# Kernel tuning notes

Hardware: AMD Instinct MI355X
Metric: run time of the kernel (lower is better)

Reference implementation:

```python
import jax, jax.numpy as jnp
import numpy as np

N_NODES = 100000
N_EDGES = 1600000
IN_FEATURES = 256
OUT_FEATURES = 64


def setup_inputs() -> dict:
    key = jax.random.key(0)
    k_x, k_r, k_c, k_v, k_w = jax.random.split(key, 5)
    x = jax.random.normal(k_x, (N_NODES, IN_FEATURES), dtype=jnp.float32)
    adj_rows = jax.random.randint(k_r, (N_EDGES,), 0, N_NODES, dtype=jnp.int64)
    adj_cols = jax.random.randint(k_c, (N_EDGES,), 0, N_NODES, dtype=jnp.int64)
    adj_vals = jax.random.uniform(k_v, (N_EDGES,), dtype=jnp.float32)
    # Glorot-uniform init as in reset_parameters()
    init_range = np.sqrt(6.0 / (IN_FEATURES + OUT_FEATURES)).astype(np.float32)
    W = jax.random.uniform(k_w, (IN_FEATURES, OUT_FEATURES), dtype=jnp.float32,
                           minval=-init_range, maxval=init_range)
    return {"x": x, "adj_rows": adj_rows, "adj_cols": adj_cols,
            "adj_vals": adj_vals, "W": W}


def reference(x, adj_rows, adj_cols, adj_vals, W):
    # support = x @ W  : dense [N, in] x [in, out]
    support = x @ W  # [N, out]
    # output = adj @ support : COO SpMM via gather + segment-sum
    # msgs[e] = adj_vals[e] * support[col[e]]
    msgs = adj_vals[:, None] * support[adj_cols]  # [E, out]
    output = jax.ops.segment_sum(msgs, adj_rows, num_segments=N_NODES)  # [N, out]
    return output
```

## Files before the change

kernel.cpp:

```cpp
#include <hip/hip_runtime.h>


#define KDIM 256
#define MDIM 64
#define BSHIFT 7
#define BMAX 1024
#define FCAP 6500

__device__ __forceinline__ void gld_lds16(const float* g, float* l) {
    __builtin_amdgcn_global_load_lds(
        (const __attribute__((address_space(1))) unsigned int*)g,
        (__attribute__((address_space(3))) unsigned int*)l, 16, 0, 0);
}

__global__ __launch_bounds__(256, 3) void gemm_xw(
    const float* __restrict__ x, const float* __restrict__ W,
    float* __restrict__ support, int nrows)
{
    __shared__ float lds[2][5120];
    const int tid  = threadIdx.x;
    const int lane = tid & 63;
    const int wid  = tid >> 6;
    const int rg   = tid >> 3;
    const int fg   = tid & 7;
    const int r0   = rg * 8;
    const int f0   = fg * 8;
    const int sk   = rg & 3;
    const int row0 = blockIdx.x * 256;

    float acc[8][8];
    #pragma unroll
    for (int i = 0; i < 8; ++i)
        #pragma unroll
        for (int j = 0; j < 8; ++j) acc[i][j] = 0.f;

    auto stage = [&](int bf, int kt) {
        #pragma unroll
        for (int j = 0; j < 4; ++j) {
            const int ig  = wid * 4 + j;
            const int row = ig * 16 + (lane >> 2);
            const int kq  = (lane & 3) ^ ((row >> 3) & 3);
            const int gr  = min(row0 + row, nrows - 1);
            gld_lds16(x + (size_t)gr * KDIM + kt + kq * 4,
                      &lds[bf][ig * 256]);
        }
        {
            const int kk = wid * 4 + (lane >> 4);
            const int fq = lane & 15;
            gld_lds16(W + (size_t)(kt + kk) * MDIM + fq * 4,
                      &lds[bf][4096 + wid * 256]);
        }
    };

    auto compute = [&](int bf) {
        const float* xs = &lds[bf][0];
        const float* ws = &lds[bf][4096];
        #pragma unroll
        for (int q = 0; q < 4; ++q) {
            float4 xv[8];
            const int slot = q ^ sk;
            #pragma unroll
            for (int i = 0; i < 8; ++i)
                xv[i] = *reinterpret_cast<const float4*>(
                            &xs[(r0 + i) * 16 + slot * 4]);
            #pragma unroll
            for (int k2 = 0; k2 < 4; ++k2) {
                const int kk = q * 4 + k2;
                const float4 wa = *reinterpret_cast<const float4*>(
                                      &ws[kk * 64 + f0]);
                const float4 wb = *reinterpret_cast<const float4*>(
                                      &ws[kk * 64 + f0 + 4]);
                #pragma unroll
                for (int i = 0; i < 8; ++i) {
                    const float xk = (k2 == 0) ? xv[i].x :
                                     (k2 == 1) ? xv[i].y :
                                     (k2 == 2) ? xv[i].z : xv[i].w;
                    acc[i][0] = fmaf(xk, wa.x, acc[i][0]);
                    acc[i][1] = fmaf(xk, wa.y, acc[i][1]);
                    acc[i][2] = fmaf(xk, wa.z, acc[i][2]);
                    acc[i][3] = fmaf(xk, wa.w, acc[i][3]);
                    acc[i][4] = fmaf(xk, wb.x, acc[i][4]);
                    acc[i][5] = fmaf(xk, wb.y, acc[i][5]);
                    acc[i][6] = fmaf(xk, wb.z, acc[i][6]);
                    acc[i][7] = fmaf(xk, wb.w, acc[i][7]);
                }
            }
        }
    };

    stage(0, 0);
    __syncthreads();
    int bf = 0;
    #pragma unroll 1
    for (int t = 0; t < KDIM / 16; ++t) {
        if (t < KDIM / 16 - 1) stage(bf ^ 1, (t + 1) * 16);
        compute(bf);
        __syncthreads();
        bf ^= 1;
    }

    #pragma unroll
    for (int i = 0; i < 8; ++i) {
        const int grow = row0 + r0 + i;
        if (grow < nrows) {
            *reinterpret_cast<float4*>(&support[(size_t)grow * MDIM + f0]) =
                make_float4(acc[i][0], acc[i][1], acc[i][2], acc[i][3]);
            *reinterpret_cast<float4*>(&support[(size_t)grow * MDIM + f0 + 4]) =
                make_float4(acc[i][4], acc[i][5], acc[i][6], acc[i][7]);
        }
    }
}

__global__ __launch_bounds__(256) void coarse_hist(
    const int* __restrict__ rows, int* __restrict__ counts,
    int nedges, int nbuckets)
{
    __shared__ int lb[BMAX];
    const int t = threadIdx.x;
    for (int i = t; i < nbuckets; i += 256) lb[i] = 0;
    __syncthreads();
    int e = blockIdx.x * 256 + t;
    const int stride = gridDim.x * 256;
    for (; e < nedges; e += stride)
        atomicAdd(&lb[rows[e] >> BSHIFT], 1);
    __syncthreads();
    for (int i = t; i < nbuckets; i += 256) {
        int c = lb[i];
        if (c) atomicAdd(&counts[i], c);
    }
}

__global__ __launch_bounds__(256) void coarse_scan(
    const int* __restrict__ counts, int* __restrict__ offsets,
    int* __restrict__ cursor, int n)
{
    __shared__ int sh[256];
    const int t = threadIdx.x;
    const int base = t * 4;
    int v0 = 0, v1 = 0, v2 = 0, v3 = 0;
    if (base + 0 < n) v0 = counts[base + 0];
    if (base + 1 < n) v1 = counts[base + 1];
    if (base + 2 < n) v2 = counts[base + 2];
    if (base + 3 < n) v3 = counts[base + 3];
    const int tsum = v0 + v1 + v2 + v3;
    sh[t] = tsum;
    __syncthreads();
    for (int off = 1; off < 256; off <<= 1) {
        int xv = (t >= off) ? sh[t - off] : 0;
        __syncthreads();
        sh[t] += xv;
        __syncthreads();
    }
    int excl = sh[t] - tsum;
    if (base + 0 < n) { offsets[base + 0] = excl; cursor[base + 0] = excl; } excl += v0;
    if (base + 1 < n) { offsets[base + 1] = excl; cursor[base + 1] = excl; } excl += v1;
    if (base + 2 < n) { offsets[base + 2] = excl; cursor[base + 2] = excl; } excl += v2;
    if (base + 3 < n) { offsets[base + 3] = excl; cursor[base + 3] = excl; }
}

__global__ __launch_bounds__(256) void bin_edges(
    const int* __restrict__ rows, const int* __restrict__ cols,
    const float* __restrict__ vals, int* __restrict__ cursor,
    int2* __restrict__ edata, int nedges, int nbuckets)
{
    __shared__ int lb[BMAX];
    const int t = threadIdx.x;
    const int per = (nedges + gridDim.x - 1) / gridDim.x;
    const int e0 = blockIdx.x * per;
    const int e1 = min(e0 + per, nedges);

    for (int i = t; i < nbuckets; i += 256) lb[i] = 0;
    __syncthreads();
    for (int e = e0 + t; e < e1; e += 256)
        atomicAdd(&lb[rows[e] >> BSHIFT], 1);
    __syncthreads();
    for (int i = t; i < nbuckets; i += 256) {
        int c = lb[i];
        lb[i] = c ? atomicAdd(&cursor[i], c) : 0;
    }
    __syncthreads();
    for (int e = e0 + t; e < e1; e += 256) {
        const int r = rows[e];
        const int pos = atomicAdd(&lb[r >> BSHIFT], 1);
        int2 pk;
        pk.x = (cols[e] & 0x1FFFF) | ((r & 127) << 17);
        pk.y = __float_as_int(vals[e]);
        edata[pos] = pk;
    }
}

__global__ __launch_bounds__(256) void fine_scatter(
    const int* __restrict__ offsets, const int* __restrict__ counts,
    int2* __restrict__ edata, int* __restrict__ foff, int* __restrict__ fcnt,
    int* __restrict__ bflag, int nrows)
{
    __shared__ int2 lrec[FCAP];
    __shared__ int cnt[128];
    __shared__ int cur[128];
    __shared__ int sh[128];
    const int t = threadIdx.x;
    const int b = blockIdx.x;
    const int beg = offsets[b];
    const int cntE = counts[b];
    const int row0 = b << BSHIFT;

    if (t < 128) cnt[t] = 0;
    __syncthreads();

    if (cntE > FCAP) {
        if (t == 0) bflag[b] = 1;
        if (t < 128) {
            const int grow = row0 + t;
            if (grow < nrows) { foff[grow] = beg; fcnt[grow] = 0; }
        }
        return;
    }

    for (int k = t; k < cntE; k += 256) {
        int2 p = edata[beg + k];
        lrec[k] = p;
        atomicAdd(&cnt[(p.x >> 17) & 127], 1);
    }
    __syncthreads();

    if (t < 128) sh[t] = cnt[t];
    __syncthreads();
    for (int off = 1; off < 128; off <<= 1) {
        int xv = 0;
        if (t < 128 && t >= off) xv = sh[t - off];
        __syncthreads();
        if (t < 128) sh[t] += xv;
        __syncthreads();
    }
    if (t < 128) {
        const int excl = sh[t] - cnt[t];
        cur[t] = excl;
        const int grow = row0 + t;
        if (grow < nrows) { foff[grow] = beg + excl; fcnt[grow] = cnt[t]; }
    }
    __syncthreads();

    for (int k = t; k < cntE; k += 256) {
        const int2 p = lrec[k];
        const int rl = (p.x >> 17) & 127;
        const int pos = beg + atomicAdd(&cur[rl], 1);
        edata[pos] = make_int2(p.x & 0x1FFFF, p.y);
    }
}

__global__ __launch_bounds__(256) void spmm_reduce(
    const int* __restrict__ foff, const int* __restrict__ fcnt,
    const int2* __restrict__ edata, const float* __restrict__ support,
    float* __restrict__ out, int nrows)
{
    const int g = blockIdx.x * 16 + (threadIdx.x >> 4);
    const int f0 = (threadIdx.x & 15) * 4;
    if (g >= nrows) return;
    int e = foff[g];
    const int end = e + fcnt[g];
    float ax = 0.f, ay = 0.f, az = 0.f, aw = 0.f;

    for (; e + 8 <= end; e += 8) {
        int2 p[8];
        #pragma unroll
        for (int u = 0; u < 8; ++u) p[u] = edata[e + u];
        float4 s[8];
        #pragma unroll
        for (int u = 0; u < 8; ++u)
            s[u] = *reinterpret_cast<const float4*>(
                       &support[(size_t)p[u].x * MDIM + f0]);
        #pragma unroll
        for (int u = 0; u < 8; ++u) {
            const float v = __int_as_float(p[u].y);
            ax = fmaf(v, s[u].x, ax); ay = fmaf(v, s[u].y, ay);
            az = fmaf(v, s[u].z, az); aw = fmaf(v, s[u].w, aw);
        }
    }
    for (; e < end; ++e) {
        const int2 p = edata[e];
        const float v = __int_as_float(p.y);
        float4 s = *reinterpret_cast<const float4*>(
                       &support[(size_t)p.x * MDIM + f0]);
        ax = fmaf(v, s.x, ax); ay = fmaf(v, s.y, ay);
        az = fmaf(v, s.z, az); aw = fmaf(v, s.w, aw);
    }
    *reinterpret_cast<float4*>(&out[(size_t)g * MDIM + f0]) =
        make_float4(ax, ay, az, aw);
}

__global__ __launch_bounds__(256) void scatter_tail(
    const int* __restrict__ offsets, const int* __restrict__ counts,
    const int* __restrict__ bflag, const int2* __restrict__ edata,
    const float* __restrict__ support, float* __restrict__ out)
{
    const int b = blockIdx.x;
    if (!bflag[b]) return;
    const int beg = offsets[b];
    const int end = beg + counts[b];
    const int row0 = b << BSHIFT;
    const int g  = threadIdx.x >> 4;
    const int f0 = (threadIdx.x & 15) * 4;
    for (int e = beg + g; e < end; e += 16) {
        const int2 p = edata[e];
        const int c = p.x & 0x1FFFF;
        const int r = row0 + ((p.x >> 17) & 127);
        const float v = __int_as_float(p.y);
        float4 s = *reinterpret_cast<const float4*>(
                       &support[(size_t)c * MDIM + f0]);
        float* op = &out[(size_t)r * MDIM + f0];
        atomicAdd(op + 0, v * s.x);
        atomicAdd(op + 1, v * s.y);
        atomicAdd(op + 2, v * s.z);
        atomicAdd(op + 3, v * s.w);
    }
}

__global__ __launch_bounds__(256) void scatter_edges(
    const int* __restrict__ rows, const int* __restrict__ cols,
    const float* __restrict__ vals, const float* __restrict__ support,
    float* __restrict__ out, int nedges)
{
    const int t = blockIdx.x * blockDim.x + threadIdx.x;
    const int fq = (t & 15) * 4;
    int e = t >> 4;
    const int estride = (gridDim.x * blockDim.x) >> 4;
    for (; e < nedges; e += estride) {
        const int r = rows[e];
        const int c = cols[e];
        const float v = vals[e];
        float4 s = *reinterpret_cast<const float4*>(
                       &support[(size_t)c * MDIM + fq]);
        float* op = &out[(size_t)r * MDIM + fq];
        atomicAdd(op + 0, v * s.x);
        atomicAdd(op + 1, v * s.y);
        atomicAdd(op + 2, v * s.z);
        atomicAdd(op + 3, v * s.w);
    }
}

extern "C" void kernel_launch(void* const* d_in, const int* in_sizes, int n_in,
                              void* d_out, int out_size, void* d_ws, size_t ws_size,
                              hipStream_t stream) {
    const float* x    = (const float*)d_in[0];
    const int*   rows = (const int*)d_in[1];
    const int*   cols = (const int*)d_in[2];
    const float* vals = (const float*)d_in[3];
    const float* W    = (const float*)d_in[4];
    float* out = (float*)d_out;

    const int nnodes = in_sizes[0] / KDIM;
    const int nedges = in_sizes[1];
    const int nbuckets = (nnodes + 127) >> BSHIFT;

    auto align256 = [](size_t v) { return (v + 255) & ~(size_t)255; };
    const size_t sz_support = align256((size_t)nnodes * MDIM * 4);
    const size_t sz_bkt     = align256((size_t)BMAX * 4);
    const size_t sz_nodes   = align256((size_t)nnodes * 4);
    const size_t sz_edata   = align256((size_t)nedges * 8);
    const size_t need = sz_support + 4 * sz_bkt + 2 * sz_nodes + sz_edata;

    char* w = (char*)d_ws;
    float* support = (float*)w;  w += sz_support;

    gemm_xw<<<dim3((nnodes + 255) / 256), dim3(256), 0, stream>>>(
        x, W, support, nnodes);

    if (ws_size >= need && nbuckets <= BMAX && nnodes <= (1 << 17)) {
        int* counts  = (int*)w;  w += sz_bkt;
        int* offsets = (int*)w;  w += sz_bkt;
        int* cursor  = (int*)w;  w += sz_bkt;
        int* bflag   = (int*)w;  w += sz_bkt;
        int* foff    = (int*)w;  w += sz_nodes;
        int* fcnt    = (int*)w;  w += sz_nodes;
        int2* edata  = (int2*)w;

        hipMemsetAsync(counts, 0, (size_t)nbuckets * 4, stream);
        hipMemsetAsync(bflag, 0, (size_t)nbuckets * 4, stream);

        coarse_hist<<<dim3(256), dim3(256), 0, stream>>>(
            rows, counts, nedges, nbuckets);
        coarse_scan<<<dim3(1), dim3(256), 0, stream>>>(
            counts, offsets, cursor, nbuckets);
        bin_edges<<<dim3(256), dim3(256), 0, stream>>>(
            rows, cols, vals, cursor, edata, nedges, nbuckets);
        fine_scatter<<<dim3(nbuckets), dim3(256), 0, stream>>>(
            offsets, counts, edata, foff, fcnt, bflag, nnodes);
        spmm_reduce<<<dim3((nnodes + 15) / 16), dim3(256), 0, stream>>>(
            foff, fcnt, edata, support, out, nnodes);
        scatter_tail<<<dim3(nbuckets), dim3(256), 0, stream>>>(
            offsets, counts, bflag, edata, support, out);
    } else {
        hipMemsetAsync(d_out, 0, (size_t)out_size * sizeof(float), stream);
        scatter_edges<<<dim3(4096), dim3(256), 0, stream>>>(
            rows, cols, vals, support, out, nedges);
    }
}
```

Before: 391.5 us.

## Replace LDS-tiled GEMM with one-row-per-thread kernel reading W uniformly

The x@W kernel changes from a 256-thread, LDS double-buffered 8x8 register-tiled design to a 64-thread kernel where each thread computes one full output row of 64 values. Each thread loads its own x row directly with float4 loads and reads W through uniform addresses, which the compiler can turn into scalar loads. This removes the LDS staging and barriers, but each thread's x reads are strided by a full row, so loads across a wavefront are uncoalesced. It also needs 64 accumulators plus prefetch registers per thread, and W rows are re-read by every wave.

```diff
diff --git a/kernel.cpp b/kernel.cpp
--- a/kernel.cpp
+++ b/kernel.cpp
@@ -7,107 +7,51 @@
 #define BMAX 1024
 #define FCAP 6500
 
-__device__ __forceinline__ void gld_lds16(const float* g, float* l) {
-    __builtin_amdgcn_global_load_lds(
-        (const __attribute__((address_space(1))) unsigned int*)g,
-        (__attribute__((address_space(3))) unsigned int*)l, 16, 0, 0);
-}
-
-__global__ __launch_bounds__(256, 3) void gemm_xw(
+__global__ __launch_bounds__(64) void gemm_xw(
     const float* __restrict__ x, const float* __restrict__ W,
     float* __restrict__ support, int nrows)
 {
-    __shared__ float lds[2][5120];
-    const int tid  = threadIdx.x;
-    const int lane = tid & 63;
-    const int wid  = tid >> 6;
-    const int rg   = tid >> 3;
-    const int fg   = tid & 7;
-    const int r0   = rg * 8;
-    const int f0   = fg * 8;
-    const int sk   = rg & 3;
-    const int row0 = blockIdx.x * 256;
-
-    float acc[8][8];
+    const int row_raw = blockIdx.x * 64 + threadIdx.x;
+    const int row = min(row_raw, nrows - 1);
+    const float4* xr = reinterpret_cast<const float4*>(x + (size_t)row * KDIM);
+
+    float acc[MDIM];
     #pragma unroll
-    for (int i = 0; i < 8; ++i)
-        #pragma unroll
-        for (int j = 0; j < 8; ++j) acc[i][j] = 0.f;
-
-    auto stage = [&](int bf, int kt) {
-        #pragma unroll
-        for (int j = 0; j < 4; ++j) {
-            const int ig  = wid * 4 + j;
-            const int row = ig * 16 + (lane >> 2);
-            const int kq  = (lane & 3) ^ ((row >> 3) & 3);
-            const int gr  = min(row0 + row, nrows - 1);
-            gld_lds16(x + (size_t)gr * KDIM + kt + kq * 4,
-                      &lds[bf][ig * 256]);
+    for (int f = 0; f < MDIM; ++f) acc[f] = 0.f;
+
+    float4 xa0 = xr[0], xa1 = xr[1], xa2 = xr[2], xa3 = xr[3];
+
+    #pragma unroll 1
+    for (int kt = 0; kt < KDIM; kt += 16) {
+        float4 xb0, xb1, xb2, xb3;
+        if (kt + 16 < KDIM) {
+            const int nq = (kt >> 2) + 4;
+            xb0 = xr[nq + 0]; xb1 = xr[nq + 1];
+            xb2 = xr[nq + 2]; xb3 = xr[nq + 3];
         }
-        {
-            const int kk = wid * 4 + (lane >> 4);
-            const int fq = lane & 15;
-            gld_lds16(W + (size_t)(kt + kk) * MDIM + fq * 4,
-                      &lds[bf][4096 + wid * 256]);
-        }
-    };
-
-    auto compute = [&](int bf) {
-        const float* xs = &lds[bf][0];
-        const float* ws = &lds[bf][4096];
         #pragma unroll
         for (int q = 0; q < 4; ++q) {
-            float4 xv[8];
-            const int slot = q ^ sk;
+            const float4 xv = (q == 0) ? xa0 : (q == 1) ? xa1 :
+                              (q == 2) ? xa2 : xa3;
             #pragma unroll
-            for (int i = 0; i < 8; ++i)
-                xv[i] = *reinterpret_cast<const float4*>(
-                            &xs[(r0 + i) * 16 + slot * 4]);
-            #pragma unroll
-            for (int k2 = 0; k2 < 4; ++k2) {
-                const int kk = q * 4 + k2;
-                const float4 wa = *reinterpret_cast<const float4*>(
-                                      &ws[kk * 64 + f0]);
-                const float4 wb = *reinterpret_cast<const float4*>(
-                                      &ws[kk * 64 + f0 + 4]);
+            for (int j = 0; j < 4; ++j) {
+                const float xk = (j == 0) ? xv.x : (j == 1) ? xv.y :
+                                 (j == 2) ? xv.z : xv.w;
+                const float* wrow = &W[(size_t)(kt + q * 4 + j) * MDIM];
                 #pragma unroll
-                for (int i = 0; i < 8; ++i) {
-                    const float xk = (k2 == 0) ? xv[i].x :
-                                     (k2 == 1) ? xv[i].y :
-                                     (k2 == 2) ? xv[i].z : xv[i].w;
-                    acc[i][0] = fmaf(xk, wa.x, acc[i][0]);
-                    acc[i][1] = fmaf(xk, wa.y, acc[i][1]);
-                    acc[i][2] = fmaf(xk, wa.z, acc[i][2]);
-                    acc[i][3] = fmaf(xk, wa.w, acc[i][3]);
-                    acc[i][4] = fmaf(xk, wb.x, acc[i][4]);
-                    acc[i][5] = fmaf(xk, wb.y, acc[i][5]);
-                    acc[i][6] = fmaf(xk, wb.z, acc[i][6]);
-                    acc[i][7] = fmaf(xk, wb.w, acc[i][7]);
-                }
+                for (int f = 0; f < MDIM; ++f)
+                    acc[f] = fmaf(xk, wrow[f], acc[f]);
             }
         }
-    };
-
-    stage(0, 0);
-    __syncthreads();
-    int bf = 0;
-    #pragma unroll 1
-    for (int t = 0; t < KDIM / 16; ++t) {
-        if (t < KDIM / 16 - 1) stage(bf ^ 1, (t + 1) * 16);
-        compute(bf);
-        __syncthreads();
-        bf ^= 1;
-    }
-
-    #pragma unroll
-    for (int i = 0; i < 8; ++i) {
-        const int grow = row0 + r0 + i;
-        if (grow < nrows) {
-            *reinterpret_cast<float4*>(&support[(size_t)grow * MDIM + f0]) =
-                make_float4(acc[i][0], acc[i][1], acc[i][2], acc[i][3]);
-            *reinterpret_cast<float4*>(&support[(size_t)grow * MDIM + f0 + 4]) =
-                make_float4(acc[i][4], acc[i][5], acc[i][6], acc[i][7]);
-        }
+        xa0 = xb0; xa1 = xb1; xa2 = xb2; xa3 = xb3;
+    }
+
+    if (row_raw < nrows) {
+        float4* o = reinterpret_cast<float4*>(support + (size_t)row * MDIM);
+        #pragma unroll
+        for (int q = 0; q < 16; ++q)
+            o[q] = make_float4(acc[q * 4 + 0], acc[q * 4 + 1],
+                               acc[q * 4 + 2], acc[q * 4 + 3]);
     }
 }
 
@@ -362,7 +306,7 @@
     char* w = (char*)d_ws;
     float* support = (float*)w;  w += sz_support;
 
-    gemm_xw<<<dim3((nnodes + 255) / 256), dim3(256), 0, stream>>>(
+    gemm_xw<<<dim3((nnodes + 63) / 64), dim3(64), 0, stream>>>(
         x, W, support, nnodes);
 
     if (ws_size >= need && nbuckets <= BMAX && nnodes <= (1 << 17)) {
```

After: 458.3 us. 17.1% more time.
